# Kernel optimization log

Measured on AMD Instinct MI355X. Metric: run time of the kernel, lower is better.

## Reference

```python
import jax, jax.numpy as jnp
import numpy as np

N, E, IN_DIM, OUT_DIM, SEM_DIM = 50000, 800000, 128, 128, 128
EPS = 1e-8


def setup_inputs() -> dict:
    key = jax.random.key(0)
    k = jax.random.split(key, 8)
    x = jax.random.normal(k[0], (N, IN_DIM), dtype=jnp.float32)
    edge_index = jax.random.randint(k[1], (2, E), 0, N, dtype=jnp.int64)
    semantic_vec = jax.random.normal(k[2], (N, SEM_DIM), dtype=jnp.float32)
    s = 1.0 / np.sqrt(IN_DIM)
    W_src = jax.random.uniform(k[3], (OUT_DIM, IN_DIM), jnp.float32, -s, s)
    b_src = jax.random.uniform(k[4], (OUT_DIM,), jnp.float32, -s, s)
    W_dst = jax.random.uniform(k[5], (OUT_DIM, IN_DIM), jnp.float32, -s, s)
    b_dst = jax.random.uniform(k[6], (OUT_DIM,), jnp.float32, -s, s)
    return {"x": x, "edge_index": edge_index, "semantic_vec": semantic_vec,
            "W_src": W_src, "b_src": b_src, "W_dst": W_dst, "b_dst": b_dst}


def _scatter_softmax(sim, dst, num_segments):
    # numerically stable segment-wise softmax over edges grouped by dst
    seg_max = jax.ops.segment_max(sim, dst, num_segments=num_segments)
    seg_max = jnp.where(jnp.isneginf(seg_max), 0.0, seg_max)
    e = jnp.exp(sim - seg_max[dst])
    seg_sum = jax.ops.segment_sum(e, dst, num_segments=num_segments)
    return e / (seg_sum[dst] + 1e-16)


def reference(x, edge_index, semantic_vec, W_src, b_src, W_dst, b_dst):
    src, dst = edge_index[0], edge_index[1]
    x_j = x[src] @ W_src.T + b_src           # [E, out_dim]
    # cosine similarity with torch eps semantics
    a = semantic_vec[src]
    b = semantic_vec[dst]
    na = jnp.maximum(jnp.linalg.norm(a, axis=-1), EPS)
    nb = jnp.maximum(jnp.linalg.norm(b, axis=-1), EPS)
    sim = jnp.sum(a * b, axis=-1) / (na * nb)  # [E]
    attn = _scatter_softmax(sim, dst, x.shape[0])
    msg = attn[:, None] * x_j                 # [E, out_dim]
    out = jax.ops.segment_sum(msg, dst, num_segments=x.shape[0])
    return out
```

## Files before the change

kernel.cpp:

```cpp
#include <hip/hip_runtime.h>
#include <hip/hip_fp16.h>

#define Nn 50000
#define Ee 800000
#define D  128
#define SLOT 64

#define B_GEMM 782
#define B_SLOT 3125
#define B_NORM 12500

struct h4 { __half2 lo, hi; };

typedef _Float16 f16x8 __attribute__((ext_vector_type(8)));
typedef float    f32x4 __attribute__((ext_vector_type(4)));

__global__ __launch_bounds__(256) void k_prep(const float* __restrict__ x,
                                              const float* __restrict__ W,
                                              const float* __restrict__ b,
                                              const int* __restrict__ ei,
                                              const float* __restrict__ sem,
                                              __half* __restrict__ y16,
                                              __half* __restrict__ sem16,
                                              int* __restrict__ cnt,
                                              int* __restrict__ slotS) {
  __shared__ __half sW[128 * 136] __attribute__((aligned(16)));
  int bid = blockIdx.x, tid = threadIdx.x;

  if (bid < B_GEMM) {
    for (int i = tid; i < 128 * 32; i += 256) {
      int r = i >> 5, c4 = (i & 31) << 2;
      float4 w = *(const float4*)(W + (size_t)r * 128 + c4);
      __half2* dst = (__half2*)&sW[r * 136 + c4];
      dst[0] = __floats2half2_rn(w.x, w.y);
      dst[1] = __floats2half2_rn(w.z, w.w);
    }
    __syncthreads();

    int wave = tid >> 6, lane = tid & 63;
    int g = lane >> 4;
    int n16 = lane & 15;
    int m0 = bid * 64 + wave * 16;
    int mA = m0 + n16; if (mA > Nn - 1) mA = Nn - 1;
    const float4* xr = (const float4*)(x + (size_t)mA * 128);

    f32x4 acc[8];
#pragma unroll
    for (int jt = 0; jt < 8; jt++) {
      float bias = b[jt * 16 + n16];
      acc[jt] = (f32x4){bias, bias, bias, bias};
    }

#pragma unroll
    for (int kt = 0; kt < 4; kt++) {
      float4 xa = xr[kt * 8 + g * 2];
      float4 xb = xr[kt * 8 + g * 2 + 1];
      f16x8 a;
      a[0] = (_Float16)xa.x; a[1] = (_Float16)xa.y; a[2] = (_Float16)xa.z; a[3] = (_Float16)xa.w;
      a[4] = (_Float16)xb.x; a[5] = (_Float16)xb.y; a[6] = (_Float16)xb.z; a[7] = (_Float16)xb.w;
#pragma unroll
      for (int jt = 0; jt < 8; jt++) {
        f16x8 bf = *(const f16x8*)(&sW[(jt * 16 + n16) * 136 + kt * 32 + g * 8]);
        acc[jt] = __builtin_amdgcn_mfma_f32_16x16x32_f16(a, bf, acc[jt], 0, 0, 0);
      }
    }

#pragma unroll
    for (int jt = 0; jt < 8; jt++) {
#pragma unroll
      for (int r = 0; r < 4; r++) {
        int row = m0 + g * 4 + r;
        if (row < Nn)
          y16[(size_t)row * 128 + jt * 16 + n16] = __float2half(acc[jt][r]);
      }
    }
  } else if (bid < B_GEMM + B_SLOT) {
    int e = (bid - B_GEMM) * 256 + tid;
    if (e < Ee) {
      int s = ei[e], d = ei[Ee + e];
      int pos = atomicAdd(cnt + d, 1);
      if (pos < SLOT)
        slotS[(size_t)d * SLOT + pos] = s;
    }
  } else {
    int n = ((bid - B_GEMM - B_SLOT) * 256 + tid) >> 6;
    int lane = tid & 63;
    if (n < Nn) {
      const float2 v = *(const float2*)(sem + (size_t)n * D + 2 * lane);
      float p = v.x * v.x + v.y * v.y;
#pragma unroll
      for (int off = 32; off > 0; off >>= 1) p += __shfl_xor(p, off);
      float inv = 1.0f / fmaxf(sqrtf(p), 1e-8f);
      *(__half2*)(sem16 + (size_t)n * D + 2 * lane) = __floats2half2_rn(v.x * inv, v.y * inv);
    }
  }
}

__global__ __launch_bounds__(256) void k_fused(const __half* __restrict__ sem16,
                                               const __half* __restrict__ y16,
                                               const int* __restrict__ slotS,
                                               const int* __restrict__ cnt,
                                               float* __restrict__ out) {
  int d = (blockIdx.x * 256 + threadIdx.x) >> 6;
  int lane = threadIdx.x & 63;
  if (d >= Nn) return;
  int sub = lane >> 5, l32 = lane & 31;
  int c = cnt[d]; if (c > SLOT) c = SLOT;

  int sv = 0;
  if (lane < c) sv = slotS[(size_t)d * SLOT + lane];

  h4 dref = ((const h4*)(sem16 + (size_t)d * D))[l32];
  float2 d0 = __half22float2(dref.lo), d1 = __half22float2(dref.hi);

  float ev = 0.0f;
  for (int i = 0; i < c; i += 4) {
    int ia = i + sub, ib = i + 2 + sub;
    int sa = __shfl(sv, ia < c ? ia : c - 1);
    int sb = __shfl(sv, ib < c ? ib : c - 1);
    h4 ra = ((const h4*)(sem16 + (size_t)sa * D))[l32];
    h4 rb = ((const h4*)(sem16 + (size_t)sb * D))[l32];
    float2 ra0 = __half22float2(ra.lo), ra1 = __half22float2(ra.hi);
    float2 rb0 = __half22float2(rb.lo), rb1 = __half22float2(rb.hi);
    float pa = d0.x * ra0.x + d0.y * ra0.y + d1.x * ra1.x + d1.y * ra1.y;
    float pb = d0.x * rb0.x + d0.y * rb0.y + d1.x * rb1.x + d1.y * rb1.y;
#pragma unroll
    for (int o = 16; o > 0; o >>= 1) { pa += __shfl_xor(pa, o); pb += __shfl_xor(pb, o); }
    float ea = expf(pa), eb = expf(pb);
    float va = __shfl(ea, (lane - i) << 5);
    float vb = __shfl(eb, (lane - i - 2) << 5);
    if (lane >= i     && lane < i + 2 && lane < c) ev = va;
    if (lane >= i + 2 && lane < i + 4 && lane < c) ev = vb;
  }

  float S = ev;
#pragma unroll
  for (int o = 32; o > 0; o >>= 1) S += __shfl_xor(S, o);
  float inv = 1.0f / (S + 1e-16f);

  float o0 = 0, o1 = 0, o2 = 0, o3 = 0;
  for (int i = 0; i < c; i += 4) {
    int ia = i + sub, ib = i + 2 + sub;
    int ca = ia < c ? ia : c - 1, cb = ib < c ? ib : c - 1;
    int sa = __shfl(sv, ca), sb = __shfl(sv, cb);
    float wa_r = __shfl(ev, ca), wb_r = __shfl(ev, cb);
    float wa = (ia < c) ? wa_r : 0.0f;
    float wb = (ib < c) ? wb_r : 0.0f;
    h4 ya = ((const h4*)(y16 + (size_t)sa * D))[l32];
    h4 yb = ((const h4*)(y16 + (size_t)sb * D))[l32];
    float2 ya0 = __half22float2(ya.lo), ya1 = __half22float2(ya.hi);
    float2 yb0 = __half22float2(yb.lo), yb1 = __half22float2(yb.hi);
    o0 += wa * ya0.x + wb * yb0.x;
    o1 += wa * ya0.y + wb * yb0.y;
    o2 += wa * ya1.x + wb * yb1.x;
    o3 += wa * ya1.y + wb * yb1.y;
  }
  o0 += __shfl_xor(o0, 32); o1 += __shfl_xor(o1, 32);
  o2 += __shfl_xor(o2, 32); o3 += __shfl_xor(o3, 32);
  if (sub == 0) {
    float4 r; r.x = o0 * inv; r.y = o1 * inv; r.z = o2 * inv; r.w = o3 * inv;
    *(float4*)(out + (size_t)d * D + l32 * 4) = r;
  }
}

extern "C" void kernel_launch(void* const* d_in, const int* in_sizes, int n_in,
                              void* d_out, int out_size, void* d_ws, size_t ws_size,
                              hipStream_t stream) {
  const float* x     = (const float*)d_in[0];
  const int*   ei    = (const int*)d_in[1];
  const float* sem   = (const float*)d_in[2];
  const float* W_src = (const float*)d_in[3];
  const float* b_src = (const float*)d_in[4];
  float* out = (float*)d_out;

  char* ws = (char*)d_ws;
  const size_t O_Y    = 0;
  const size_t O_S16  = 12800000;
  const size_t O_CNT  = 25600000;
  const size_t O_SS   = 25800000;
  const size_t NEED   = 38600000;
  if (ws_size < NEED) return;

  __half* y16   = (__half*)(ws + O_Y);
  __half* sem16 = (__half*)(ws + O_S16);
  int* cnt   = (int*)(ws + O_CNT);
  int* slotS = (int*)(ws + O_SS);

  hipMemsetAsync(cnt, 0, Nn * sizeof(int), stream);
  k_prep<<<B_GEMM + B_SLOT + B_NORM, 256, 0, stream>>>(x, W_src, b_src, ei, sem,
                                                       y16, sem16, cnt, slotS);
  k_fused<<<(Nn + 3) / 4, 256, 0, stream>>>(sem16, y16, slotS, cnt, out);
}
```

Baseline: 228.5 us.

## Split GEMM into separate kernel with LDS-staged A tile; coarsen scatter and norm blocks

Moves the x·W GEMM out of the combined prep kernel into its own launch, which stages the 64-row x tile in shared memory as fp16 before the MFMA loop instead of having each lane load and convert its own A fragment. The slot-scatter and semantic-normalize work goes into a second kernel where each thread handles two edges and each block normalizes 16 rows, cutting block count. This adds an extra kernel launch and serializes the GEMM with the scatter/norm work, which previously ran concurrently in one grid, while the larger per-block LDS footprint lowers GEMM occupancy.

```diff
diff --git a/kernel.cpp b/kernel.cpp
--- a/kernel.cpp
+++ b/kernel.cpp
@@ -6,86 +6,99 @@
 #define D  128
 #define SLOT 64
 
-#define B_GEMM 782
-#define B_SLOT 3125
-#define B_NORM 12500
+#define B_SCAT 1563
+#define B_NORM 3125
 
 struct h4 { __half2 lo, hi; };
 
 typedef _Float16 f16x8 __attribute__((ext_vector_type(8)));
 typedef float    f32x4 __attribute__((ext_vector_type(4)));
 
-__global__ __launch_bounds__(256) void k_prep(const float* __restrict__ x,
+__global__ __launch_bounds__(256) void k_gemm(const float* __restrict__ x,
                                               const float* __restrict__ W,
                                               const float* __restrict__ b,
-                                              const int* __restrict__ ei,
-                                              const float* __restrict__ sem,
-                                              __half* __restrict__ y16,
-                                              __half* __restrict__ sem16,
-                                              int* __restrict__ cnt,
-                                              int* __restrict__ slotS) {
-  __shared__ __half sW[128 * 136] __attribute__((aligned(16)));
+                                              __half* __restrict__ y16) {
+  __shared__ __half sW16[128 * 136] __attribute__((aligned(16)));
+  __shared__ __half sA16[64 * 136]  __attribute__((aligned(16)));
   int bid = blockIdx.x, tid = threadIdx.x;
-
-  if (bid < B_GEMM) {
-    for (int i = tid; i < 128 * 32; i += 256) {
-      int r = i >> 5, c4 = (i & 31) << 2;
-      float4 w = *(const float4*)(W + (size_t)r * 128 + c4);
-      __half2* dst = (__half2*)&sW[r * 136 + c4];
-      dst[0] = __floats2half2_rn(w.x, w.y);
-      dst[1] = __floats2half2_rn(w.z, w.w);
-    }
-    __syncthreads();
-
+  int n0 = bid * 64;
+
+  for (int r = 0; r < 16; r++) {
+    int i = tid + 256 * r;
+    int row = i >> 5, c4 = (i & 31) << 2;
+    float4 w = *(const float4*)(W + (size_t)row * 128 + c4);
+    __half2* dst = (__half2*)&sW16[row * 136 + c4];
+    dst[0] = __floats2half2_rn(w.x, w.y);
+    dst[1] = __floats2half2_rn(w.z, w.w);
+  }
+  for (int r = 0; r < 8; r++) {
+    int i = tid + 256 * r;
+    int row = i >> 5, c4 = (i & 31) << 2;
+    int nr = n0 + row; if (nr >= Nn) nr = Nn - 1;
+    float4 v = *(const float4*)(x + (size_t)nr * 128 + c4);
+    __half2* dst = (__half2*)&sA16[row * 136 + c4];
+    dst[0] = __floats2half2_rn(v.x, v.y);
+    dst[1] = __floats2half2_rn(v.z, v.w);
+  }
+  __syncthreads();
+
+  int wave = tid >> 6, lane = tid & 63;
+  int g = lane >> 4;
+  int n16 = lane & 15;
+  int m0 = n0 + wave * 16;
+
+  f32x4 acc[8];
+#pragma unroll
+  for (int jt = 0; jt < 8; jt++) {
+    float bias = b[jt * 16 + n16];
+    acc[jt] = (f32x4){bias, bias, bias, bias};
+  }
+
+#pragma unroll
+  for (int kt = 0; kt < 4; kt++) {
+    f16x8 a = *(const f16x8*)(&sA16[(wave * 16 + n16) * 136 + kt * 32 + g * 8]);
+#pragma unroll
+    for (int jt = 0; jt < 8; jt++) {
+      f16x8 bf = *(const f16x8*)(&sW16[(jt * 16 + n16) * 136 + kt * 32 + g * 8]);
+      acc[jt] = __builtin_amdgcn_mfma_f32_16x16x32_f16(a, bf, acc[jt], 0, 0, 0);
+    }
+  }
+
+#pragma unroll
+  for (int jt = 0; jt < 8; jt++) {
+#pragma unroll
+    for (int r = 0; r < 4; r++) {
+      int row = m0 + g * 4 + r;
+      if (row < Nn)
+        y16[(size_t)row * 128 + jt * 16 + n16] = __float2half(acc[jt][r]);
+    }
+  }
+}
+
+__global__ __launch_bounds__(256) void k_prep2(const int* __restrict__ ei,
+                                               const float* __restrict__ sem,
+                                               __half* __restrict__ sem16,
+                                               int* __restrict__ cnt,
+                                               int* __restrict__ slotS) {
+  int bid = blockIdx.x, tid = threadIdx.x;
+  if (bid < B_SCAT) {
+    int base = bid * 512 + tid;
+#pragma unroll
+    for (int u = 0; u < 2; u++) {
+      int e = base + u * 256;
+      if (e < Ee) {
+        int s = ei[e], d = ei[Ee + e];
+        int pos = atomicAdd(cnt + d, 1);
+        if (pos < SLOT)
+          slotS[(size_t)d * SLOT + pos] = s;
+      }
+    }
+  } else {
+    int nb = (bid - B_SCAT) * 16;
     int wave = tid >> 6, lane = tid & 63;
-    int g = lane >> 4;
-    int n16 = lane & 15;
-    int m0 = bid * 64 + wave * 16;
-    int mA = m0 + n16; if (mA > Nn - 1) mA = Nn - 1;
-    const float4* xr = (const float4*)(x + (size_t)mA * 128);
-
-    f32x4 acc[8];
-#pragma unroll
-    for (int jt = 0; jt < 8; jt++) {
-      float bias = b[jt * 16 + n16];
-      acc[jt] = (f32x4){bias, bias, bias, bias};
-    }
-
-#pragma unroll
-    for (int kt = 0; kt < 4; kt++) {
-      float4 xa = xr[kt * 8 + g * 2];
-      float4 xb = xr[kt * 8 + g * 2 + 1];
-      f16x8 a;
-      a[0] = (_Float16)xa.x; a[1] = (_Float16)xa.y; a[2] = (_Float16)xa.z; a[3] = (_Float16)xa.w;
-      a[4] = (_Float16)xb.x; a[5] = (_Float16)xb.y; a[6] = (_Float16)xb.z; a[7] = (_Float16)xb.w;
-#pragma unroll
-      for (int jt = 0; jt < 8; jt++) {
-        f16x8 bf = *(const f16x8*)(&sW[(jt * 16 + n16) * 136 + kt * 32 + g * 8]);
-        acc[jt] = __builtin_amdgcn_mfma_f32_16x16x32_f16(a, bf, acc[jt], 0, 0, 0);
-      }
-    }
-
-#pragma unroll
-    for (int jt = 0; jt < 8; jt++) {
-#pragma unroll
-      for (int r = 0; r < 4; r++) {
-        int row = m0 + g * 4 + r;
-        if (row < Nn)
-          y16[(size_t)row * 128 + jt * 16 + n16] = __float2half(acc[jt][r]);
-      }
-    }
-  } else if (bid < B_GEMM + B_SLOT) {
-    int e = (bid - B_GEMM) * 256 + tid;
-    if (e < Ee) {
-      int s = ei[e], d = ei[Ee + e];
-      int pos = atomicAdd(cnt + d, 1);
-      if (pos < SLOT)
-        slotS[(size_t)d * SLOT + pos] = s;
-    }
-  } else {
-    int n = ((bid - B_GEMM - B_SLOT) * 256 + tid) >> 6;
-    int lane = tid & 63;
-    if (n < Nn) {
+#pragma unroll
+    for (int it = 0; it < 4; it++) {
+      int n = nb + it * 4 + wave;
       const float2 v = *(const float2*)(sem + (size_t)n * D + 2 * lane);
       float p = v.x * v.x + v.y * v.y;
 #pragma unroll
@@ -107,8 +120,7 @@
   int sub = lane >> 5, l32 = lane & 31;
   int c = cnt[d]; if (c > SLOT) c = SLOT;
 
-  int sv = 0;
-  if (lane < c) sv = slotS[(size_t)d * SLOT + lane];
+  int sv = (lane < c) ? slotS[(size_t)d * SLOT + lane] : 0;
 
   h4 dref = ((const h4*)(sem16 + (size_t)d * D))[l32];
   float2 d0 = __half22float2(dref.lo), d1 = __half22float2(dref.hi);
@@ -148,12 +160,12 @@
     float wb = (ib < c) ? wb_r : 0.0f;
     h4 ya = ((const h4*)(y16 + (size_t)sa * D))[l32];
     h4 yb = ((const h4*)(y16 + (size_t)sb * D))[l32];
-    float2 ya0 = __half22float2(ya.lo), ya1 = __half22float2(ya.hi);
-    float2 yb0 = __half22float2(yb.lo), yb1 = __half22float2(yb.hi);
-    o0 += wa * ya0.x + wb * yb0.x;
-    o1 += wa * ya0.y + wb * yb0.y;
-    o2 += wa * ya1.x + wb * yb1.x;
-    o3 += wa * ya1.y + wb * yb1.y;
+    float2 a0 = __half22float2(ya.lo), a1 = __half22float2(ya.hi);
+    float2 b0 = __half22float2(yb.lo), b1 = __half22float2(yb.hi);
+    o0 += wa * a0.x + wb * b0.x;
+    o1 += wa * a0.y + wb * b0.y;
+    o2 += wa * a1.x + wb * b1.x;
+    o3 += wa * a1.y + wb * b1.y;
   }
   o0 += __shfl_xor(o0, 32); o1 += __shfl_xor(o1, 32);
   o2 += __shfl_xor(o2, 32); o3 += __shfl_xor(o3, 32);
@@ -187,7 +199,7 @@
   int* slotS = (int*)(ws + O_SS);
 
   hipMemsetAsync(cnt, 0, Nn * sizeof(int), stream);
-  k_prep<<<B_GEMM + B_SLOT + B_NORM, 256, 0, stream>>>(x, W_src, b_src, ei, sem,
-                                                       y16, sem16, cnt, slotS);
+  k_gemm<<<(Nn + 63) / 64, 256, 0, stream>>>(x, W_src, b_src, y16);
+  k_prep2<<<B_SCAT + B_NORM, 256, 0, stream>>>(ei, sem, sem16, cnt, slotS);
   k_fused<<<(Nn + 3) / 4, 256, 0, stream>>>(sem16, y16, slotS, cnt, out);
 }
```

New measurement: 220.7 us. 3.4% less time.
